# Optimization experiments

Measured on AMD Instinct MI355X. Metric: run time of the kernel, lower is better.

Reference implementation:

```python
import jax, jax.numpy as jnp
import numpy as np

B, H, W, C, HEADS = 4, 64, 64, 512, 8
HD = C // HEADS
L = H * W
BIAS_LEVEL = 0.1
LN_EPS = 1e-5


def _ln(x, g, b):
    mu = jnp.mean(x, axis=-1, keepdims=True)
    var = jnp.var(x, axis=-1, keepdims=True)
    return (x - mu) * jax.lax.rsqrt(var + LN_EPS) * g + b


def setup_inputs() -> dict:
    key = jax.random.key(0)
    ks = jax.random.split(key, 16)
    s = 0.02
    return {
        "x": jax.random.normal(ks[0], (B, L, C), jnp.float32),
        "rpe": jax.random.normal(ks[1], (H, HEADS, W, W), jnp.float32),
        "qkv_w": jax.random.normal(ks[2], (3 * C, C), jnp.float32) * s,
        "proj_w": jax.random.normal(ks[3], (C, C), jnp.float32) * s,
        "proj_b": jnp.zeros((C,), jnp.float32),
        "norm1_w": jnp.ones((C,), jnp.float32),
        "norm1_b": jnp.zeros((C,), jnp.float32),
        "norm2_w": jnp.ones((C,), jnp.float32),
        "norm2_b": jnp.zeros((C,), jnp.float32),
        "fc1_w": jax.random.normal(ks[4], (4 * C, C), jnp.float32) * s,
        "fc1_b": jnp.zeros((4 * C,), jnp.float32),
        "fc2_w": jax.random.normal(ks[5], (C, 4 * C), jnp.float32) * s,
        "fc2_b": jnp.zeros((C,), jnp.float32),
    }


def reference(x, rpe, qkv_w, proj_w, proj_b, norm1_w, norm1_b, norm2_w, norm2_b,
              fc1_w, fc1_b, fc2_w, fc2_b):
    # --- qkv projection ---
    img = _ln(x, norm1_w, norm1_b)
    qkv = (img @ qkv_w.T).reshape(B, L, 3, C)
    q, k, v = qkv[:, :, 0], qkv[:, :, 1], qkv[:, :, 2]

    # idx=0 horizontal windows: each row of the HxW grid is a window of len W.
    def to_win(t):  # (B, L, C) -> (B*H, heads, W, hd)
        return t.reshape(B * H, W, HEADS, HD).transpose(0, 2, 1, 3)

    qw, kw, vw = to_win(q), to_win(k), to_win(v)

    # attention scores + relative position bias (RPE tiled over batch)
    attn = jnp.einsum('whqd,whkd->whqk', qw, kw)
    attn = attn + BIAS_LEVEL * jnp.tile(rpe, (B, 1, 1, 1))

    # magnitude gate M per window
    M = jnp.mean(jnp.abs(attn), axis=(1, 2, 3), keepdims=True)  # (B*H,1,1,1)
    M = M / jnp.max(M)
    M = jnp.maximum(M, 0.5)

    # cosine-based score transform: 1 - cos(pi/2 * l2normalize(attn))
    nrm = jnp.maximum(jnp.linalg.norm(attn, axis=-1, keepdims=True), 1e-12)
    attn = 1.0 - jnp.cos((attn / nrm) * (jnp.pi / 2.0))
    attn = attn * M

    o = jnp.einsum('whqk,whkd->whqd', attn, vw)  # (B*H, heads, W, hd)
    o = o.transpose(0, 2, 1, 3).reshape(B, L, C)

    # residual gating by (1 - M)
    res = (x.reshape(B * H, 1, W, C) * (1.0 - M)).reshape(B, L, C)
    attened = o + res

    attened = attened @ proj_w.T + proj_b
    x1 = x + attened

    h = _ln(x1, norm2_w, norm2_b)
    h = jax.nn.gelu(h @ fc1_w.T + fc1_b, approximate=False)
    h = h @ fc2_w.T + fc2_b
    return x1 + h
```

## Files before the change

### kernel.cpp

```cpp
#include <hip/hip_runtime.h>
#include <hip/hip_bf16.h>
#include <math.h>

typedef unsigned short u16;
typedef __bf16 bf16x8 __attribute__((ext_vector_type(8)));
typedef float f32x4 __attribute__((ext_vector_type(4)));
typedef unsigned short u16x8 __attribute__((ext_vector_type(8)));

typedef const __attribute__((address_space(1))) void* gas_ptr;
typedef __attribute__((address_space(3))) void* las_ptr;

__device__ __forceinline__ float bf2f(u16 u) {
    union { unsigned int i; float f; } x;
    x.i = ((unsigned int)u) << 16;
    return x.f;
}
__device__ __forceinline__ u16 f2bf(float f) {
    __hip_bfloat16 h = __float2bfloat16(f);
    return __builtin_bit_cast(u16, h);
}
__device__ __forceinline__ __bf16 f2bfr(float f) {
    __hip_bfloat16 h = __float2bfloat16(f);
    return __builtin_bit_cast(__bf16, h);
}
__device__ __forceinline__ void load_lds16(const void* g, void* l) {
    __builtin_amdgcn_global_load_lds((gas_ptr)g, (las_ptr)l, 16, 0, 0);
}
__device__ __forceinline__ float gelu_f(float v) {
    const float a = fabsf(v) * 0.70710678118654752f;
    const float tt = 1.0f / fmaf(0.3275911f, a, 1.0f);
    float poly = fmaf(tt, 1.061405429f, -1.453152027f);
    poly = fmaf(tt, poly, 1.421413741f);
    poly = fmaf(tt, poly, -0.284496736f);
    poly = fmaf(tt, poly, 0.254829592f);
    const float erfa = 1.0f - poly * tt * __expf(-a * a);
    const float erfv = copysignf(erfa, v);
    return 0.5f * v * (1.0f + erfv);
}

__global__ __launch_bounds__(256) void cvt_all_k(const float* __restrict__ qkv_w,
                                                 const float* __restrict__ proj_w,
                                                 const float* __restrict__ fc1w,
                                                 const float* __restrict__ fc2w,
                                                 u16* __restrict__ wqkv,
                                                 u16* __restrict__ wproj,
                                                 u16* __restrict__ wfc1,
                                                 u16* __restrict__ wfc2) {
    const int b = blockIdx.x;
    const float* src; u16* dst; int off;
    if (b < 768)       { src = qkv_w;  dst = wqkv;  off = b; }
    else if (b < 1024) { src = proj_w; dst = wproj; off = b - 768; }
    else if (b < 2048) { src = fc1w;   dst = wfc1;  off = b - 1024; }
    else               { src = fc2w;   dst = wfc2;  off = b - 2048; }
    const int i = off * 256 + threadIdx.x;
    const float4 v = ((const float4*)src)[i];
    ushort4 o;
    o.x = f2bf(v.x); o.y = f2bf(v.y); o.z = f2bf(v.z); o.w = f2bf(v.w);
    ((ushort4*)dst)[i] = o;
}

__global__ __launch_bounds__(256) void ln_row_k(const float* __restrict__ x,
                                                const float* __restrict__ gw,
                                                const float* __restrict__ gb,
                                                u16* __restrict__ outp) {
    const int row = blockIdx.x * 4 + (threadIdx.x >> 6);
    const int lane = threadIdx.x & 63;
    const float* rp = x + (size_t)row * 512 + lane * 8;
    const float4 a = *(const float4*)rp;
    const float4 b = *(const float4*)(rp + 4);
    float s = a.x + a.y + a.z + a.w + b.x + b.y + b.z + b.w;
    float q = a.x*a.x + a.y*a.y + a.z*a.z + a.w*a.w
            + b.x*b.x + b.y*b.y + b.z*b.z + b.w*b.w;
    #pragma unroll
    for (int o = 1; o < 64; o <<= 1) {
        s += __shfl_xor(s, o);
        q += __shfl_xor(q, o);
    }
    const float mean = s * (1.0f / 512.0f);
    const float var = q * (1.0f / 512.0f) - mean * mean;
    const float rstd = rsqrtf(var + 1e-5f);
    const float4 g0 = *(const float4*)(gw + lane * 8);
    const float4 g1 = *(const float4*)(gw + lane * 8 + 4);
    const float4 c0 = *(const float4*)(gb + lane * 8);
    const float4 c1 = *(const float4*)(gb + lane * 8 + 4);
    u16x8 o16;
    o16[0] = f2bf((a.x - mean) * rstd * g0.x + c0.x);
    o16[1] = f2bf((a.y - mean) * rstd * g0.y + c0.y);
    o16[2] = f2bf((a.z - mean) * rstd * g0.z + c0.z);
    o16[3] = f2bf((a.w - mean) * rstd * g0.w + c0.w);
    o16[4] = f2bf((b.x - mean) * rstd * g1.x + c1.x);
    o16[5] = f2bf((b.y - mean) * rstd * g1.y + c1.y);
    o16[6] = f2bf((b.z - mean) * rstd * g1.z + c1.z);
    o16[7] = f2bf((b.w - mean) * rstd * g1.w + c1.w);
    *(u16x8*)(outp + (size_t)row * 512 + lane * 8) = o16;
}

__global__ __launch_bounds__(256) void ln2stat_k(const float* __restrict__ statP,
                                                 float* __restrict__ lnst) {
    const int row = blockIdx.x * 256 + threadIdx.x;
    const float4* p = (const float4*)(statP + (size_t)row * 16);
    const float4 a = p[0], b = p[1], c = p[2], d = p[3];
    const float s = a.x + a.z + b.x + b.z + c.x + c.z + d.x + d.z;
    const float q = a.y + a.w + b.y + b.w + c.y + c.w + d.y + d.w;
    const float mean = s * (1.0f / 512.0f);
    const float var = q * (1.0f / 512.0f) - mean * mean;
    ((float2*)lnst)[row] = make_float2(mean, rsqrtf(var + 1e-5f));
}

template<int EPI, int AFUSE>
__global__ __launch_bounds__(256) void gemm_bt(const u16* __restrict__ A,
                                               const u16* __restrict__ W,
                                               const float* __restrict__ bias,
                                               const float* __restrict__ res_f,
                                               const u16* __restrict__ res_bf,
                                               void* __restrict__ outp,
                                               int M, int N, int K,
                                               const float* __restrict__ aM,
                                               const u16* __restrict__ aO,
                                               const float* __restrict__ aX,
                                               float* __restrict__ statP,
                                               const float* __restrict__ lnst,
                                               const float* __restrict__ lngw,
                                               const float* __restrict__ lngb) {
    __shared__ __bf16 As[2][128 * 64];
    __shared__ __bf16 Bs[2][128 * 64];
    const int t = threadIdx.x;
    const int l = t & 63;
    const int w = t >> 6;
    const int wm = w & 1, wn = w >> 1;
    const int bm = blockIdx.x * 128, bn = blockIdx.y * 128;
    const int r = l & 15, g4 = l >> 4;

    f32x4 acc[4][4] = {};

    const int rowS = t >> 3;
    const int cS = (t & 7) ^ (rowS & 7);
    const size_t rstep = (size_t)32 * K;
    const u16* wBase = W + (size_t)(bn + rowS) * K + cS * 8;
    const u16* aBase = A + (size_t)(bm + rowS) * K + cS * 8;
    const size_t afBase = (size_t)(bm + rowS) * K + cS * 8;

    float Mw[4], lnmean[4], lnrstd[4];
    if (AFUSE == 1) {
        #pragma unroll
        for (int j = 0; j < 4; ++j) Mw[j] = aM[(bm + rowS + 32 * j) >> 6];
    } else if (AFUSE == 2) {
        #pragma unroll
        for (int j = 0; j < 4; ++j) {
            const float2 st = ((const float2*)lnst)[bm + rowS + 32 * j];
            lnmean[j] = st.x; lnrstd[j] = st.y;
        }
    }

    auto stage = [&](int buf, int kt) {
        float gwv[8], gbv[8];
        if (AFUSE == 2) {
            const int kc = kt + cS * 8;
            *(float4*)&gwv[0] = *(const float4*)(lngw + kc);
            *(float4*)&gwv[4] = *(const float4*)(lngw + kc + 4);
            *(float4*)&gbv[0] = *(const float4*)(lngb + kc);
            *(float4*)&gbv[4] = *(const float4*)(lngb + kc + 4);
        }
        #pragma unroll
        for (int j = 0; j < 4; ++j) {
            if (AFUSE == 1) {
                const size_t gidx = afBase + j * rstep + kt;
                const float rf = 1.0f - Mw[j];
                const u16x8 ov = *(const u16x8*)(aO + gidx);
                const float4 x0 = *(const float4*)(aX + gidx);
                const float4 x1 = *(const float4*)(aX + gidx + 4);
                bf16x8 val;
                val[0] = f2bfr(Mw[j] * bf2f(ov[0]) + rf * x0.x);
                val[1] = f2bfr(Mw[j] * bf2f(ov[1]) + rf * x0.y);
                val[2] = f2bfr(Mw[j] * bf2f(ov[2]) + rf * x0.z);
                val[3] = f2bfr(Mw[j] * bf2f(ov[3]) + rf * x0.w);
                val[4] = f2bfr(Mw[j] * bf2f(ov[4]) + rf * x1.x);
                val[5] = f2bfr(Mw[j] * bf2f(ov[5]) + rf * x1.y);
                val[6] = f2bfr(Mw[j] * bf2f(ov[6]) + rf * x1.z);
                val[7] = f2bfr(Mw[j] * bf2f(ov[7]) + rf * x1.w);
                *(bf16x8*)&As[buf][(j * 256 + t) * 8] = val;
            } else if (AFUSE == 2) {
                const size_t gidx = afBase + j * rstep + kt;
                const u16x8 xv = *(const u16x8*)(A + gidx);
                bf16x8 val;
                #pragma unroll
                for (int e = 0; e < 8; ++e)
                    val[e] = f2bfr((bf2f(xv[e]) - lnmean[j]) * lnrstd[j] * gwv[e] + gbv[e]);
                *(bf16x8*)&As[buf][(j * 256 + t) * 8] = val;
            } else {
                load_lds16(aBase + j * rstep + kt, &As[buf][(j * 256 + t) * 8]);
            }
            load_lds16(wBase + j * rstep + kt, &Bs[buf][(j * 256 + t) * 8]);
        }
    };

    const int nk = K >> 6;
    stage(0, 0);
    __syncthreads();
    for (int s = 0; s < nk; ++s) {
        if (s + 1 < nk) stage((s + 1) & 1, (s + 1) << 6);
        const int buf = s & 1;
        bf16x8 af[4][2], bfr[4][2];
        #pragma unroll
        for (int i = 0; i < 4; ++i) {
            const int ra = wm * 64 + i * 16 + r;
            const int rb = wn * 64 + i * 16 + r;
            #pragma unroll
            for (int h = 0; h < 2; ++h) {
                af[i][h]  = *(const bf16x8*)&As[buf][ra * 64 + (((h * 4 + g4) ^ (ra & 7)) << 3)];
                bfr[i][h] = *(const bf16x8*)&Bs[buf][rb * 64 + (((h * 4 + g4) ^ (rb & 7)) << 3)];
            }
        }
        #pragma unroll
        for (int i = 0; i < 4; ++i)
            #pragma unroll
            for (int j = 0; j < 4; ++j)
                #pragma unroll
                for (int h = 0; h < 2; ++h)
                    acc[i][j] = __builtin_amdgcn_mfma_f32_16x16x32_bf16(
                        af[i][h], bfr[j][h], acc[i][j], 0, 0, 0);
        __syncthreads();
    }

    #pragma unroll
    for (int i = 0; i < 4; ++i) {
        #pragma unroll
        for (int rr = 0; rr < 4; ++rr) {
            const int m = bm + wm * 64 + i * 16 + g4 * 4 + rr;
            float s = 0.f, q = 0.f;
            #pragma unroll
            for (int j = 0; j < 4; ++j) {
                const int n = bn + wn * 64 + j * 16 + r;
                float v = acc[i][j][rr];
                const size_t idx = (size_t)m * N + n;
                if (EPI == 0) {
                    ((u16*)outp)[idx] = f2bf(v);
                } else if (EPI == 1) {
                    v += bias[n] + res_f[idx];
                    ((u16*)outp)[idx] = f2bf(v);
                    s += v; q += v * v;
                } else if (EPI == 2) {
                    ((u16*)outp)[idx] = f2bf(gelu_f(v + bias[n]));
                } else {
                    ((float*)outp)[idx] = v + bias[n] + bf2f(res_bf[idx]);
                }
            }
            if (EPI == 1) {
                #pragma unroll
                for (int o = 1; o < 16; o <<= 1) {
                    s += __shfl_xor(s, o);
                    q += __shfl_xor(q, o);
                }
                if (r == 0)
                    ((float2*)statP)[(size_t)m * 8 + blockIdx.y * 2 + wn] =
                        make_float2(s, q);
            }
        }
    }
}

__global__ __launch_bounds__(256) void attn_k(const u16* __restrict__ qkv,
                                              const float* __restrict__ rpe,
                                              float* __restrict__ Mpart,
                                              u16* __restrict__ Obuf) {
    const int blk = blockIdx.x;
    const int wh = blk >> 3, head = blk & 7;
    const int himg = wh & 63;
    const int t = threadIdx.x, l = t & 63, w = t >> 6;
    __shared__ __bf16 Qs[4096];
    __shared__ __bf16 Ks[4096];
    __shared__ __bf16 Vt[4096];
    __shared__ __bf16 Ps[4096];
    __shared__ float red[4];

    #pragma unroll
    for (int p = 0; p < 2; ++p) {
        const int sb = (p * 256 + t) << 4;
        const int row = sb >> 7;
        const int gl = ((sb >> 4) & 7) ^ (row & 7);
        const size_t gsrc = (size_t)(wh * 64 + row) * 1536 + head * 64 + gl * 8;
        const int lbase = p * 2048 + w * 512;
        load_lds16(qkv + gsrc, &Qs[lbase]);
        load_lds16(qkv + gsrc + 512, &Ks[lbase]);
    }
    {
        const int k = t >> 2, dc = (t & 3) * 16;
        const u16* vr = qkv + (size_t)(wh * 64 + k) * 1536 + 1024 + head * 64 + dc;
        u16x8 v0 = *(const u16x8*)vr;
        u16x8 v1 = *(const u16x8*)(vr + 8);
        const int g = k >> 3, klo = k & 7;
        #pragma unroll
        for (int i = 0; i < 8; ++i) {
            const int d0 = dc + i, d1 = dc + 8 + i;
            Vt[d0 * 64 + ((g ^ (d0 & 7)) << 3) + klo] = __builtin_bit_cast(__bf16, (u16)v0[i]);
            Vt[d1 * 64 + ((g ^ (d1 & 7)) << 3) + klo] = __builtin_bit_cast(__bf16, (u16)v1[i]);
        }
    }
    __syncthreads();

    const int r = l & 15, g4 = l >> 4;
    f32x4 acc[4] = {};
    #pragma unroll
    for (int h = 0; h < 2; ++h) {
        const int rowq = w * 16 + r;
        bf16x8 aq = *(const bf16x8*)&Qs[rowq * 64 + (((h * 4 + g4) ^ (rowq & 7)) << 3)];
        #pragma unroll
        for (int j = 0; j < 4; ++j) {
            const int rowk = j * 16 + r;
            bf16x8 bk = *(const bf16x8*)&Ks[rowk * 64 + (((h * 4 + g4) ^ (rowk & 7)) << 3)];
            acc[j] = __builtin_amdgcn_mfma_f32_16x16x32_bf16(aq, bk, acc[j], 0, 0, 0);
        }
    }

    float v[4][4];
    float asum = 0.f;
    float ss[4] = {0.f, 0.f, 0.f, 0.f};
    const size_t rpe_base = (size_t)(himg * 8 + head) * 4096 + (size_t)(w * 16 + g4 * 4) * 64 + r;
    #pragma unroll
    for (int j = 0; j < 4; ++j) {
        #pragma unroll
        for (int rr = 0; rr < 4; ++rr) {
            const float val = acc[j][rr] + 0.1f * rpe[rpe_base + rr * 64 + j * 16];
            v[j][rr] = val;
            asum += fabsf(val);
            ss[rr] += val * val;
        }
    }
    #pragma unroll
    for (int m = 1; m < 16; m <<= 1) {
        #pragma unroll
        for (int rr = 0; rr < 4; ++rr) ss[rr] += __shfl_xor(ss[rr], m);
    }
    float srev[4];
    #pragma unroll
    for (int rr = 0; rr < 4; ++rr)
        srev[rr] = 0.25f / fmaxf(sqrtf(ss[rr]), 1e-12f);

    #pragma unroll
    for (int j = 0; j < 4; ++j) {
        #pragma unroll
        for (int rr = 0; rr < 4; ++rr) {
            const float pv = 1.0f - __builtin_amdgcn_cosf(v[j][rr] * srev[rr]);
            const int rl = g4 * 4 + rr;
            const int c = j * 16 + r;
            Ps[w * 1024 + rl * 64 + (((c >> 3) ^ (rl & 7)) << 3) + (c & 7)] = f2bfr(pv);
        }
    }

    f32x4 oacc[4] = {};
    #pragma unroll
    for (int ks = 0; ks < 2; ++ks) {
        const int ga = ks * 4 + g4;
        bf16x8 pa = *(const bf16x8*)&Ps[w * 1024 + r * 64 + ((ga ^ (r & 7)) << 3)];
        #pragma unroll
        for (int j = 0; j < 4; ++j) {
            const int d = j * 16 + r;
            bf16x8 vb = *(const bf16x8*)&Vt[d * 64 + ((ga ^ (d & 7)) << 3)];
            oacc[j] = __builtin_amdgcn_mfma_f32_16x16x32_bf16(pa, vb, oacc[j], 0, 0, 0);
        }
    }

    #pragma unroll
    for (int j = 0; j < 4; ++j) {
        #pragma unroll
        for (int rr = 0; rr < 4; ++rr) {
            const int token = wh * 64 + w * 16 + g4 * 4 + rr;
            Obuf[(size_t)token * 512 + head * 64 + j * 16 + r] = f2bf(oacc[j][rr]);
        }
    }

    #pragma unroll
    for (int o = 1; o < 64; o <<= 1) asum += __shfl_xor(asum, o);
    if (l == 0) red[w] = asum;
    __syncthreads();
    if (t == 0) Mpart[blk] = red[0] + red[1] + red[2] + red[3];
}

__global__ __launch_bounds__(256) void mfinal_k(const float* __restrict__ Mpart,
                                                float* __restrict__ M) {
    const int t = threadIdx.x;
    float m = 0.f;
    #pragma unroll
    for (int h = 0; h < 8; ++h) m += Mpart[t * 8 + h];
    m *= (1.0f / 32768.0f);
    float mx = m;
    #pragma unroll
    for (int o = 1; o < 64; o <<= 1) mx = fmaxf(mx, __shfl_xor(mx, o));
    __shared__ float red[4];
    if ((t & 63) == 0) red[t >> 6] = mx;
    __syncthreads();
    mx = fmaxf(fmaxf(red[0], red[1]), fmaxf(red[2], red[3]));
    M[t] = fmaxf(m / mx, 0.5f);
}

extern "C" void kernel_launch(void* const* d_in, const int* in_sizes, int n_in,
                              void* d_out, int out_size, void* d_ws, size_t ws_size,
                              hipStream_t stream) {
    (void)in_sizes; (void)n_in; (void)out_size; (void)ws_size;
    const float* x      = (const float*)d_in[0];
    const float* rpe    = (const float*)d_in[1];
    const float* qkv_w  = (const float*)d_in[2];
    const float* proj_w = (const float*)d_in[3];
    const float* proj_b = (const float*)d_in[4];
    const float* n1w    = (const float*)d_in[5];
    const float* n1b    = (const float*)d_in[6];
    const float* n2w    = (const float*)d_in[7];
    const float* n2b    = (const float*)d_in[8];
    const float* fc1w   = (const float*)d_in[9];
    const float* fc1b   = (const float*)d_in[10];
    const float* fc2w   = (const float*)d_in[11];
    const float* fc2b   = (const float*)d_in[12];
    float* out = (float*)d_out;

    char* ws = (char*)d_ws;
    float* Mpart = (float*)ws;
    float* Mbuf  = (float*)(ws + 8192);
    u16* wqkv  = (u16*)(ws + 16384);
    u16* wproj = (u16*)(ws + 16384 + 1572864);
    u16* wfc1  = (u16*)(ws + 16384 + 2097152);
    u16* wfc2  = (u16*)(ws + 16384 + 4194304);
    u16* bufA  = (u16*)(ws + 6307840);
    float* statP = (float*)(ws + 23085056);
    float* lnst  = (float*)(ws + 23085056 + 1048576);
    char* R    = ws + 39862272;
    u16*   qkvb = (u16*)R;
    u16*   Obuf = (u16*)(R + 50331648);
    u16*   gbuf = (u16*)R;

    cvt_all_k<<<3072, 256, 0, stream>>>(qkv_w, proj_w, fc1w, fc2w,
                                        wqkv, wproj, wfc1, wfc2);
    ln_row_k<<<4096, 256, 0, stream>>>(x, n1w, n1b, bufA);
    gemm_bt<0, 0><<<dim3(128, 12), 256, 0, stream>>>(
        bufA, wqkv, nullptr, nullptr, nullptr, qkvb, 16384, 1536, 512,
        nullptr, nullptr, nullptr, nullptr, nullptr, nullptr, nullptr);
    attn_k<<<2048, 256, 0, stream>>>(qkvb, rpe, Mpart, Obuf);
    mfinal_k<<<1, 256, 0, stream>>>(Mpart, Mbuf);
    gemm_bt<1, 1><<<dim3(128, 4), 256, 0, stream>>>(
        Obuf, wproj, proj_b, x, nullptr, bufA, 16384, 512, 512,
        Mbuf, Obuf, x, statP, nullptr, nullptr, nullptr);
    ln2stat_k<<<64, 256, 0, stream>>>(statP, lnst);
    gemm_bt<2, 2><<<dim3(128, 16), 256, 0, stream>>>(
        bufA, wfc1, fc1b, nullptr, nullptr, gbuf, 16384, 2048, 512,
        nullptr, nullptr, nullptr, nullptr, lnst, n2w, n2b);
    gemm_bt<3, 0><<<dim3(128, 4), 256, 0, stream>>>(
        gbuf, wfc2, fc2b, nullptr, bufA, out, 16384, 512, 2048,
        nullptr, nullptr, nullptr, nullptr, nullptr, nullptr, nullptr);
}
```

Before: 206.6 us.

## Unfuse LN2 into standalone row kernel and software-pipeline fused A loads

The LayerNorm-2 prologue fused into the fc1 GEMM's A-tile staging is removed. A separate row LayerNorm kernel now normalizes the bf16 x1 into a new buffer, and fc1 uses the plain async LDS load path. The proj-GEMM epilogue stops computing per-row partial stats. The AFUSE=1 path now splits global loads and LDS writes around the MFMA compute to overlap load latency. The trade is an extra kernel launch and an extra 16 MB bf16 round trip, in exchange for removing redundant per-tile LN math across the 16 N-blocks of fc1.

```diff
diff --git a/kernel.cpp b/kernel.cpp
--- a/kernel.cpp
+++ b/kernel.cpp
@@ -95,16 +95,42 @@
     *(u16x8*)(outp + (size_t)row * 512 + lane * 8) = o16;
 }
 
-__global__ __launch_bounds__(256) void ln2stat_k(const float* __restrict__ statP,
-                                                 float* __restrict__ lnst) {
-    const int row = blockIdx.x * 256 + threadIdx.x;
-    const float4* p = (const float4*)(statP + (size_t)row * 16);
-    const float4 a = p[0], b = p[1], c = p[2], d = p[3];
-    const float s = a.x + a.z + b.x + b.z + c.x + c.z + d.x + d.z;
-    const float q = a.y + a.w + b.y + b.w + c.y + c.w + d.y + d.w;
+__global__ __launch_bounds__(256) void ln_row_bf_k(const u16* __restrict__ x1,
+                                                   const float* __restrict__ gw,
+                                                   const float* __restrict__ gb,
+                                                   u16* __restrict__ outp) {
+    const int row = blockIdx.x * 4 + (threadIdx.x >> 6);
+    const int lane = threadIdx.x & 63;
+    const u16x8 v = *(const u16x8*)(x1 + (size_t)row * 512 + lane * 8);
+    float f[8];
+    float s = 0.f, q = 0.f;
+    #pragma unroll
+    for (int e = 0; e < 8; ++e) {
+        f[e] = bf2f(v[e]);
+        s += f[e]; q += f[e] * f[e];
+    }
+    #pragma unroll
+    for (int o = 1; o < 64; o <<= 1) {
+        s += __shfl_xor(s, o);
+        q += __shfl_xor(q, o);
+    }
     const float mean = s * (1.0f / 512.0f);
     const float var = q * (1.0f / 512.0f) - mean * mean;
-    ((float2*)lnst)[row] = make_float2(mean, rsqrtf(var + 1e-5f));
+    const float rstd = rsqrtf(var + 1e-5f);
+    const float4 g0 = *(const float4*)(gw + lane * 8);
+    const float4 g1 = *(const float4*)(gw + lane * 8 + 4);
+    const float4 c0 = *(const float4*)(gb + lane * 8);
+    const float4 c1 = *(const float4*)(gb + lane * 8 + 4);
+    u16x8 o16;
+    o16[0] = f2bf((f[0] - mean) * rstd * g0.x + c0.x);
+    o16[1] = f2bf((f[1] - mean) * rstd * g0.y + c0.y);
+    o16[2] = f2bf((f[2] - mean) * rstd * g0.z + c0.z);
+    o16[3] = f2bf((f[3] - mean) * rstd * g0.w + c0.w);
+    o16[4] = f2bf((f[4] - mean) * rstd * g1.x + c1.x);
+    o16[5] = f2bf((f[5] - mean) * rstd * g1.y + c1.y);
+    o16[6] = f2bf((f[6] - mean) * rstd * g1.z + c1.z);
+    o16[7] = f2bf((f[7] - mean) * rstd * g1.w + c1.w);
+    *(u16x8*)(outp + (size_t)row * 512 + lane * 8) = o16;
 }
 
 template<int EPI, int AFUSE>
@@ -117,11 +143,7 @@
                                                int M, int N, int K,
                                                const float* __restrict__ aM,
                                                const u16* __restrict__ aO,
-                                               const float* __restrict__ aX,
-                                               float* __restrict__ statP,
-                                               const float* __restrict__ lnst,
-                                               const float* __restrict__ lngw,
-                                               const float* __restrict__ lngb) {
+                                               const float* __restrict__ aX) {
     __shared__ __bf16 As[2][128 * 64];
     __shared__ __bf16 Bs[2][128 * 64];
     const int t = threadIdx.x;
@@ -140,66 +162,51 @@
     const u16* aBase = A + (size_t)(bm + rowS) * K + cS * 8;
     const size_t afBase = (size_t)(bm + rowS) * K + cS * 8;
 
-    float Mw[4], lnmean[4], lnrstd[4];
+    float Mw[4];
     if (AFUSE == 1) {
         #pragma unroll
         for (int j = 0; j < 4; ++j) Mw[j] = aM[(bm + rowS + 32 * j) >> 6];
-    } else if (AFUSE == 2) {
+    }
+
+    u16x8 ovr[4];
+    float4 x0r[4], x1r[4];
+
+    auto loadA = [&](int kt) __attribute__((always_inline)) {
         #pragma unroll
         for (int j = 0; j < 4; ++j) {
-            const float2 st = ((const float2*)lnst)[bm + rowS + 32 * j];
-            lnmean[j] = st.x; lnrstd[j] = st.y;
-        }
-    }
-
-    auto stage = [&](int buf, int kt) {
-        float gwv[8], gbv[8];
-        if (AFUSE == 2) {
-            const int kc = kt + cS * 8;
-            *(float4*)&gwv[0] = *(const float4*)(lngw + kc);
-            *(float4*)&gwv[4] = *(const float4*)(lngw + kc + 4);
-            *(float4*)&gbv[0] = *(const float4*)(lngb + kc);
-            *(float4*)&gbv[4] = *(const float4*)(lngb + kc + 4);
-        }
+            const size_t gidx = afBase + j * rstep + kt;
+            ovr[j] = *(const u16x8*)(aO + gidx);
+            x0r[j] = *(const float4*)(aX + gidx);
+            x1r[j] = *(const float4*)(aX + gidx + 4);
+        }
+    };
+    auto writeA = [&](int buf) __attribute__((always_inline)) {
         #pragma unroll
         for (int j = 0; j < 4; ++j) {
-            if (AFUSE == 1) {
-                const size_t gidx = afBase + j * rstep + kt;
-                const float rf = 1.0f - Mw[j];
-                const u16x8 ov = *(const u16x8*)(aO + gidx);
-                const float4 x0 = *(const float4*)(aX + gidx);
-                const float4 x1 = *(const float4*)(aX + gidx + 4);
-                bf16x8 val;
-                val[0] = f2bfr(Mw[j] * bf2f(ov[0]) + rf * x0.x);
-                val[1] = f2bfr(Mw[j] * bf2f(ov[1]) + rf * x0.y);
-                val[2] = f2bfr(Mw[j] * bf2f(ov[2]) + rf * x0.z);
-                val[3] = f2bfr(Mw[j] * bf2f(ov[3]) + rf * x0.w);
-                val[4] = f2bfr(Mw[j] * bf2f(ov[4]) + rf * x1.x);
-                val[5] = f2bfr(Mw[j] * bf2f(ov[5]) + rf * x1.y);
-                val[6] = f2bfr(Mw[j] * bf2f(ov[6]) + rf * x1.z);
-                val[7] = f2bfr(Mw[j] * bf2f(ov[7]) + rf * x1.w);
-                *(bf16x8*)&As[buf][(j * 256 + t) * 8] = val;
-            } else if (AFUSE == 2) {
-                const size_t gidx = afBase + j * rstep + kt;
-                const u16x8 xv = *(const u16x8*)(A + gidx);
-                bf16x8 val;
-                #pragma unroll
-                for (int e = 0; e < 8; ++e)
-                    val[e] = f2bfr((bf2f(xv[e]) - lnmean[j]) * lnrstd[j] * gwv[e] + gbv[e]);
-                *(bf16x8*)&As[buf][(j * 256 + t) * 8] = val;
-            } else {
-                load_lds16(aBase + j * rstep + kt, &As[buf][(j * 256 + t) * 8]);
-            }
+            const float rf = 1.0f - Mw[j];
+            bf16x8 val;
+            val[0] = f2bfr(Mw[j] * bf2f(ovr[j][0]) + rf * x0r[j].x);
+            val[1] = f2bfr(Mw[j] * bf2f(ovr[j][1]) + rf * x0r[j].y);
+            val[2] = f2bfr(Mw[j] * bf2f(ovr[j][2]) + rf * x0r[j].z);
+            val[3] = f2bfr(Mw[j] * bf2f(ovr[j][3]) + rf * x0r[j].w);
+            val[4] = f2bfr(Mw[j] * bf2f(ovr[j][4]) + rf * x1r[j].x);
+            val[5] = f2bfr(Mw[j] * bf2f(ovr[j][5]) + rf * x1r[j].y);
+            val[6] = f2bfr(Mw[j] * bf2f(ovr[j][6]) + rf * x1r[j].z);
+            val[7] = f2bfr(Mw[j] * bf2f(ovr[j][7]) + rf * x1r[j].w);
+            *(bf16x8*)&As[buf][(j * 256 + t) * 8] = val;
+        }
+    };
+    auto stageA_g = [&](int buf, int kt) __attribute__((always_inline)) {
+        #pragma unroll
+        for (int j = 0; j < 4; ++j)
+            load_lds16(aBase + j * rstep + kt, &As[buf][(j * 256 + t) * 8]);
+    };
+    auto stageB = [&](int buf, int kt) __attribute__((always_inline)) {
+        #pragma unroll
+        for (int j = 0; j < 4; ++j)
             load_lds16(wBase + j * rstep + kt, &Bs[buf][(j * 256 + t) * 8]);
-        }
     };
-
-    const int nk = K >> 6;
-    stage(0, 0);
-    __syncthreads();
-    for (int s = 0; s < nk; ++s) {
-        if (s + 1 < nk) stage((s + 1) & 1, (s + 1) << 6);
-        const int buf = s & 1;
+    auto compute = [&](int buf) __attribute__((always_inline)) {
         bf16x8 af[4][2], bfr[4][2];
         #pragma unroll
         for (int i = 0; i < 4; ++i) {
@@ -219,41 +226,44 @@
                 for (int h = 0; h < 2; ++h)
                     acc[i][j] = __builtin_amdgcn_mfma_f32_16x16x32_bf16(
                         af[i][h], bfr[j][h], acc[i][j], 0, 0, 0);
+    };
+
+    const int nk = K >> 6;
+    if (AFUSE == 1) { loadA(0); writeA(0); }
+    else            stageA_g(0, 0);
+    stageB(0, 0);
+    __syncthreads();
+    for (int s = 0; s < nk; ++s) {
+        const int nb = (s + 1) & 1;
+        if (s + 1 < nk) {
+            if (AFUSE == 1) loadA((s + 1) << 6);
+            else            stageA_g(nb, (s + 1) << 6);
+            stageB(nb, (s + 1) << 6);
+        }
+        compute(s & 1);
+        if (AFUSE == 1 && s + 1 < nk) writeA(nb);
         __syncthreads();
     }
 
     #pragma unroll
     for (int i = 0; i < 4; ++i) {
         #pragma unroll
-        for (int rr = 0; rr < 4; ++rr) {
-            const int m = bm + wm * 64 + i * 16 + g4 * 4 + rr;
-            float s = 0.f, q = 0.f;
+        for (int j = 0; j < 4; ++j) {
             #pragma unroll
-            for (int j = 0; j < 4; ++j) {
+            for (int rr = 0; rr < 4; ++rr) {
+                const int m = bm + wm * 64 + i * 16 + g4 * 4 + rr;
                 const int n = bn + wn * 64 + j * 16 + r;
                 float v = acc[i][j][rr];
                 const size_t idx = (size_t)m * N + n;
                 if (EPI == 0) {
                     ((u16*)outp)[idx] = f2bf(v);
                 } else if (EPI == 1) {
-                    v += bias[n] + res_f[idx];
-                    ((u16*)outp)[idx] = f2bf(v);
-                    s += v; q += v * v;
+                    ((u16*)outp)[idx] = f2bf(v + bias[n] + res_f[idx]);
                 } else if (EPI == 2) {
                     ((u16*)outp)[idx] = f2bf(gelu_f(v + bias[n]));
                 } else {
                     ((float*)outp)[idx] = v + bias[n] + bf2f(res_bf[idx]);
                 }
-            }
-            if (EPI == 1) {
-                #pragma unroll
-                for (int o = 1; o < 16; o <<= 1) {
-                    s += __shfl_xor(s, o);
-                    q += __shfl_xor(q, o);
-                }
-                if (r == 0)
-                    ((float2*)statP)[(size_t)m * 8 + blockIdx.y * 2 + wn] =
-                        make_float2(s, q);
             }
         }
     }
@@ -420,8 +430,7 @@
     u16* wfc1  = (u16*)(ws + 16384 + 2097152);
     u16* wfc2  = (u16*)(ws + 16384 + 4194304);
     u16* bufA  = (u16*)(ws + 6307840);
-    float* statP = (float*)(ws + 23085056);
-    float* lnst  = (float*)(ws + 23085056 + 1048576);
+    u16* bufB  = (u16*)(ws + 23085056);
     char* R    = ws + 39862272;
     u16*   qkvb = (u16*)R;
     u16*   Obuf = (u16*)(R + 50331648);
@@ -432,17 +441,17 @@
     ln_row_k<<<4096, 256, 0, stream>>>(x, n1w, n1b, bufA);
     gemm_bt<0, 0><<<dim3(128, 12), 256, 0, stream>>>(
         bufA, wqkv, nullptr, nullptr, nullptr, qkvb, 16384, 1536, 512,
-        nullptr, nullptr, nullptr, nullptr, nullptr, nullptr, nullptr);
+        nullptr, nullptr, nullptr);
     attn_k<<<2048, 256, 0, stream>>>(qkvb, rpe, Mpart, Obuf);
     mfinal_k<<<1, 256, 0, stream>>>(Mpart, Mbuf);
     gemm_bt<1, 1><<<dim3(128, 4), 256, 0, stream>>>(
         Obuf, wproj, proj_b, x, nullptr, bufA, 16384, 512, 512,
-        Mbuf, Obuf, x, statP, nullptr, nullptr, nullptr);
-    ln2stat_k<<<64, 256, 0, stream>>>(statP, lnst);
-    gemm_bt<2, 2><<<dim3(128, 16), 256, 0, stream>>>(
-        bufA, wfc1, fc1b, nullptr, nullptr, gbuf, 16384, 2048, 512,
-        nullptr, nullptr, nullptr, nullptr, lnst, n2w, n2b);
+        Mbuf, Obuf, x);
+    ln_row_bf_k<<<4096, 256, 0, stream>>>(bufA, n2w, n2b, bufB);
+    gemm_bt<2, 0><<<dim3(128, 16), 256, 0, stream>>>(
+        bufB, wfc1, fc1b, nullptr, nullptr, gbuf, 16384, 2048, 512,
+        nullptr, nullptr, nullptr);
     gemm_bt<3, 0><<<dim3(128, 4), 256, 0, stream>>>(
         gbuf, wfc2, fc2b, nullptr, bufA, out, 16384, 512, 2048,
-        nullptr, nullptr, nullptr, nullptr, nullptr, nullptr, nullptr);
-}
+        nullptr, nullptr, nullptr);
+}
```

Result: no change. 205.1 us (-0.7%).
